# Kernel tuning notes

Hardware: AMD Instinct MI355X
Metric: run time of the kernel (lower is better)

The kernel has to match this reference:

```python
import jax, jax.numpy as jnp
import numpy as np
from jax import lax

B, H, W, C = 4, 96, 96, 256
F = 256
KH = KW = 3
K = KH * KW
DG = 1
CG = C // DG
SH = SW = 1
DH = DW = 1
PAD_T = (DH * (KH - 1)) // 2  # 'same' padding (top/left) for 3x3 dil 1
PAD_L = (DW * (KW - 1)) // 2


def setup_inputs() -> dict:
    key = jax.random.key(0)
    k1, k2, k3 = jax.random.split(key, 3)
    x = jax.random.normal(k1, (B, H, W, C), jnp.float32)
    # offset/mask conv weights (orig init zeros; small random to exercise sampling)
    om_kernel = jax.random.normal(k2, (KH, KW, C, DG * 3 * K), jnp.float32) * 0.01
    om_bias = jnp.zeros((DG * 3 * K,), jnp.float32)
    stdv = 1.0 / np.sqrt(C * KH * KW)
    kernel = jax.random.uniform(k3, (K * C, F), jnp.float32, -stdv, stdv)
    bias = jnp.zeros((F,), jnp.float32)
    return {"x": x, "om_kernel": om_kernel, "om_bias": om_bias, "kernel": kernel, "bias": bias}


def reference(x, om_kernel, om_bias, kernel, bias):
    Bx, Hx, Wx, Cx = x.shape
    # offset/mask prediction conv (NHWC, 'SAME', matches keras Conv2D)
    om = lax.conv_general_dilated(
        x, om_kernel, (SH, SW), "SAME", rhs_dilation=(DH, DW),
        dimension_numbers=("NHWC", "HWIO", "NHWC")) + om_bias
    Ho, Wo = om.shape[1], om.shape[2]
    off = om[..., : 2 * DG * K].reshape(Bx, Ho, Wo, DG, K, 2)  # (dy, dx) per group/kpoint
    mask = jax.nn.sigmoid(om[..., 2 * DG * K :]).reshape(Bx, Ho, Wo, DG, K) * 2.0

    # base sampling grid: y = ho*SH - PAD_T + ki*DH (+ dy), similarly x
    base_y = (jnp.arange(Ho) * SH - PAD_T)[:, None] + (jnp.arange(KH) * DH)[None, :]  # [Ho,KH]
    base_x = (jnp.arange(Wo) * SW - PAD_L)[:, None] + (jnp.arange(KW) * DW)[None, :]  # [Wo,KW]
    gy = jnp.broadcast_to(base_y[:, None, :, None], (Ho, Wo, KH, KW)).reshape(Ho, Wo, K)
    gx = jnp.broadcast_to(base_x[None, :, None, :], (Ho, Wo, KH, KW)).reshape(Ho, Wo, K)

    py = gy[None, :, :, None, :].astype(x.dtype) + off[..., 0]  # [B,Ho,Wo,DG,K]
    px = gx[None, :, :, None, :].astype(x.dtype) + off[..., 1]

    # reorder to [B, N, DG] with N = Ho*Wo*K (K varies fastest after spatial)
    N = Ho * Wo * K
    py = py.transpose(0, 1, 2, 4, 3).reshape(Bx, N, DG)
    px = px.transpose(0, 1, 2, 4, 3).reshape(Bx, N, DG)
    mask_t = mask.transpose(0, 1, 2, 4, 3).reshape(Bx, N, DG)

    y0 = jnp.floor(py)
    x0 = jnp.floor(px)
    fy = py - y0
    fx = px - x0

    xf = x.reshape(Bx, Hx * Wx, DG, CG)
    val = jnp.zeros((Bx, N, DG, CG), x.dtype)
    for yi, wy in ((y0, 1.0 - fy), (y0 + 1.0, fy)):
        for xi, wx in ((x0, 1.0 - fx), (x0 + 1.0, fx)):
            valid = (yi >= 0) & (yi < Hx) & (xi >= 0) & (xi < Wx)
            yc = jnp.clip(yi, 0, Hx - 1).astype(jnp.int32)
            xc = jnp.clip(xi, 0, Wx - 1).astype(jnp.int32)
            lin = yc * Wx + xc  # [B,N,DG]
            g = jnp.take_along_axis(xf, lin[..., None], axis=1)  # [B,N,DG,CG]
            val = val + g * (wy * wx * valid.astype(x.dtype))[..., None]

    # modulate and im2col -> GEMM
    cols = (val * mask_t[..., None]).reshape(Bx, Ho * Wo, K * Cx)
    out = jnp.matmul(cols, kernel).reshape(Bx, Ho, Wo, -1) + bias
    return out
```

## Files before the change

kernel.cpp:

```cpp
#include <hip/hip_runtime.h>
#include <hip/hip_bf16.h>
#include <stdint.h>
#include <stddef.h>


namespace {
constexpr int H  = 96, W = 96, C = 256, F = 256;
constexpr int HP = 98;
constexpr int NP = 4 * 96 * 96;
constexpr int KC = 9 * 256;

constexpr int NB_PAD  = 4 * HP * HP / 8;
constexpr int NB_OMW  = 9 * 32;
constexpr int NB_WT   = (KC / 64) * (F / 64);
}

typedef __attribute__((ext_vector_type(8))) short bf16x8;
typedef __attribute__((ext_vector_type(4))) float floatx4;

__device__ __forceinline__ void load_lds16(const void* g, void* l) {
  __builtin_amdgcn_global_load_lds((const __attribute__((address_space(1))) void*)g,
                                   (__attribute__((address_space(3))) void*)l,
                                   16, 0, 0);
}

__device__ __forceinline__ uint32_t pk2(float lo, float hi) {
  __hip_bfloat162 t = __float22bfloat162_rn(float2{lo, hi});
  return *reinterpret_cast<uint32_t*>(&t);
}

__device__ __forceinline__ void acc8(uint4 v, float w, float* a) {
  a[0] += w * __uint_as_float(v.x << 16); a[1] += w * __uint_as_float(v.x & 0xffff0000u);
  a[2] += w * __uint_as_float(v.y << 16); a[3] += w * __uint_as_float(v.y & 0xffff0000u);
  a[4] += w * __uint_as_float(v.z << 16); a[5] += w * __uint_as_float(v.z & 0xffff0000u);
  a[6] += w * __uint_as_float(v.w << 16); a[7] += w * __uint_as_float(v.w & 0xffff0000u);
}

__global__ __launch_bounds__(256) void k_pad(const float* __restrict__ x,
                                             uint4* __restrict__ xp4) {
  const int tid = threadIdx.x;
  const int sub = tid >> 5, cid = tid & 31;
  const int pp  = blockIdx.x * 8 + sub;
  const int b   = pp / (HP * HP);
  const int r   = pp % (HP * HP);
  const int y   = r / HP, xq = r % HP;
  uint4 o = {0u, 0u, 0u, 0u};
  if (y >= 1 && y <= H && xq >= 1 && xq <= W) {
    const float* src = x + ((size_t)((b * H + (y - 1)) * W + (xq - 1))) * C + cid * 8;
    const float4 v0 = *(const float4*)src;
    const float4 v1 = *(const float4*)(src + 4);
    o.x = pk2(v0.x, v0.y); o.y = pk2(v0.z, v0.w);
    o.z = pk2(v1.x, v1.y); o.w = pk2(v1.z, v1.w);
  }
  xp4[(size_t)pp * 32 + cid] = o;
}

__global__ __launch_bounds__(256) void k_wprep(const float* __restrict__ omk,
                                               const float* __restrict__ kern,
                                               __hip_bfloat16* __restrict__ wom,
                                               __hip_bfloat16* __restrict__ wt) {
  __shared__ float t[64][65];
  const int bi = blockIdx.x, tid = threadIdx.x;

  if (bi < NB_OMW) {
    const int kk = bi / 32, oc = bi % 32;
    float v = (oc < 27) ? omk[(size_t)(kk * 256 + tid) * 27 + oc] : 0.f;
    wom[(size_t)oc * KC + kk * 256 + tid] = __float2bfloat16(v);
  } else {
    const int j   = bi - NB_OMW;
    const int kc0 = (j % (KC / 64)) * 64, f0 = (j / (KC / 64)) * 64;
    const int rr = tid >> 6, cc = tid & 63;
#pragma unroll
    for (int i = 0; i < 16; ++i)
      t[rr * 16 + i][cc] = kern[(size_t)(kc0 + rr * 16 + i) * F + f0 + cc];
    __syncthreads();
#pragma unroll
    for (int i = 0; i < 16; ++i) {
      const int frow = rr * 16 + i;
      wt[(size_t)(f0 + frow) * KC + kc0 + cc] = __float2bfloat16(t[cc][frow]);
    }
  }
}

__global__ __launch_bounds__(256) void k_omgemm(const __hip_bfloat16* __restrict__ xp,
                                                const __hip_bfloat16* __restrict__ wom,
                                                float* __restrict__ pOm) {
  __shared__ __align__(16) char lds[12288];
  const int tid  = threadIdx.x;
  const int xr   = blockIdx.x;
  const int xs   = (xr & 7) * 72 + (xr >> 3);
  const int m0   = xs * 64;
  const int lane = tid & 63, wave = tid >> 6;
  const int quad = lane >> 4, l16 = lane & 15;

  const int kp  = (tid & 3) ^ ((tid >> 3) & 3);
  const int row = tid >> 2;
  {
  }
  const int p  = m0 + row;
  const int b  = p / (H * W);
  const int hw = p % (H * W);
  const int h  = hw / W, w = hw % W;
  const __hip_bfloat16* abase = xp + ((size_t)(b * HP + h) * HP + w) * C + kp * 8;
  const __hip_bfloat16* bbase = wom + (size_t)row * KC + kp * 8;

  auto stage = [&](int buf, int k0) {
    const int kk = k0 >> 8, c0 = k0 & 255;
    const int aoff = ((kk / 3) * HP + (kk % 3)) * C + c0;
    char* base = &lds[buf * 6144];
    load_lds16(abase + aoff, base + tid * 16);
    if (tid < 128) load_lds16(bbase + k0, base + 4096 + tid * 16);
  };

  floatx4 acc[2];
  acc[0] = (floatx4){0.f, 0.f, 0.f, 0.f};
  acc[1] = (floatx4){0.f, 0.f, 0.f, 0.f};

  const int swq = (quad ^ ((l16 >> 1) & 3)) * 16;

  stage(0, 0);
  int cur = 0;
#pragma unroll 1
  for (int k0 = 0; k0 < KC; k0 += 32) {
    __syncthreads();
    if (k0 + 32 < KC) stage(cur ^ 1, k0 + 32);
    const char* base = &lds[cur * 6144];

    bf16x8 af = *(const bf16x8*)&base[(wave * 16 + l16) * 64 + swq];
    bf16x8 b0 = *(const bf16x8*)&base[4096 + (l16) * 64 + swq];
    bf16x8 b1 = *(const bf16x8*)&base[4096 + (16 + l16) * 64 + swq];
    acc[0] = __builtin_amdgcn_mfma_f32_16x16x32_bf16(af, b0, acc[0], 0, 0, 0);
    acc[1] = __builtin_amdgcn_mfma_f32_16x16x32_bf16(af, b1, acc[1], 0, 0, 0);
    cur ^= 1;
  }

#pragma unroll
  for (int nt = 0; nt < 2; ++nt) {
    const int gm = m0 + wave * 16 + quad * 4;
    const int gn = nt * 16 + l16;
#pragma unroll
    for (int r = 0; r < 4; ++r)
      pOm[(size_t)(gm + r) * 32 + gn] = acc[nt][r];
  }
}

__global__ __launch_bounds__(256) void k_sample(const uint4* __restrict__ xp4,
                                                const float* __restrict__ pOm,
                                                const float* __restrict__ om_bias,
                                                uint4* __restrict__ cols4) {
  __shared__ float2 s_ow[8][9][4];

  const int tid = threadIdx.x;
  const int sub = tid >> 5, cid = tid & 31;
  const int bs  = (blockIdx.x & 7) * 576 + (blockIdx.x >> 3);

  if (tid < 72) {
    const int ps = tid / 9, k = tid % 9;
    const int p  = bs * 8 + ps;
    const int b  = p / (H * W);
    const int hw = p % (H * W);
    const int h = hw / W, w = hw % W;
    const float dy = om_bias[2 * k]     + pOm[(size_t)p * 32 + 2 * k];
    const float dx = om_bias[2 * k + 1] + pOm[(size_t)p * 32 + 2 * k + 1];
    const float mv = om_bias[18 + k]    + pOm[(size_t)p * 32 + 18 + k];
    const float m  = 2.f / (1.f + __expf(-mv));
    const float sy = (float)(h - 1 + k / 3) + dy;
    const float sx = (float)(w - 1 + k % 3) + dx;
    const float y0f = floorf(sy), x0f = floorf(sx);
    const float fy = sy - y0f, fx = sx - x0f;
    const int y0 = (int)y0f, x0 = (int)x0f;
#pragma unroll
    for (int c2 = 0; c2 < 4; ++c2) {
      const int dy2 = c2 >> 1, dx2 = c2 & 1;
      const int yi = y0 + dy2, xi = x0 + dx2;
      const bool valid = (yi >= 0) & (yi < H) & (xi >= 0) & (xi < W);
      const float wgt = valid ? (dy2 ? fy : 1.f - fy) * (dx2 ? fx : 1.f - fx) * m : 0.f;
      const int yc = min(max(yi + 1, 0), HP - 1);
      const int xc = min(max(xi + 1, 0), HP - 1);
      const int off = ((b * HP + yc) * HP + xc) * 32;
      s_ow[ps][k][c2] = float2{__int_as_float(off), wgt};
    }
  }
  __syncthreads();

  const int p = bs * 8 + sub;
  uint4* __restrict__ ob = cols4 + (size_t)p * 288 + cid;

#pragma unroll 1
  for (int k = 0; k < 9; ++k) {
    const float2 ow0 = s_ow[sub][k][0], ow1 = s_ow[sub][k][1];
    const float2 ow2 = s_ow[sub][k][2], ow3 = s_ow[sub][k][3];
    float a[8] = {0.f, 0.f, 0.f, 0.f, 0.f, 0.f, 0.f, 0.f};
    acc8(xp4[(size_t)__float_as_int(ow0.x) + cid], ow0.y, a);
    acc8(xp4[(size_t)__float_as_int(ow1.x) + cid], ow1.y, a);
    acc8(xp4[(size_t)__float_as_int(ow2.x) + cid], ow2.y, a);
    acc8(xp4[(size_t)__float_as_int(ow3.x) + cid], ow3.y, a);
    uint4 o;
    o.x = pk2(a[0], a[1]); o.y = pk2(a[2], a[3]);
    o.z = pk2(a[4], a[5]); o.w = pk2(a[6], a[7]);
    ob[k * 32] = o;
  }
}

__global__ __launch_bounds__(256) void k_gemm(const __hip_bfloat16* __restrict__ A,
                                              const __hip_bfloat16* __restrict__ Bt,
                                              const float* __restrict__ bias,
                                              float* __restrict__ out) {
  __shared__ __align__(16) char lds[28672];

  const int tid  = threadIdx.x;
  const int m0   = blockIdx.x * 96;
  const int n0   = blockIdx.y * 128;
  const int lane = tid & 63, wave = tid >> 6;
  const int wm = wave & 1, wn = wave >> 1;
  const int quad = lane >> 4, l16 = lane & 15;

  const int row = tid >> 2, kp = (tid & 3) ^ ((tid >> 3) & 3);
  const __hip_bfloat16* a0 = A  + (size_t)(m0 + row) * KC + kp * 8;
  const __hip_bfloat16* a1 = A  + (size_t)(m0 + 64 + row) * KC + kp * 8;
  const __hip_bfloat16* b0 = Bt + (size_t)(n0 + row) * KC + kp * 8;
  const __hip_bfloat16* b1 = Bt + (size_t)(n0 + 64 + row) * KC + kp * 8;

  auto stage = [&](int buf, int k0) {
    char* base = &lds[buf * 14336];
    load_lds16(a0 + k0, base + tid * 16);
    if (tid < 128) load_lds16(a1 + k0, base + 4096 + tid * 16);
    load_lds16(b0 + k0, base + 6144 + tid * 16);
    load_lds16(b1 + k0, base + 10240 + tid * 16);
  };

  floatx4 acc[3][4];
#pragma unroll
  for (int i = 0; i < 3; ++i)
#pragma unroll
    for (int j = 0; j < 4; ++j) acc[i][j] = (floatx4){0.f, 0.f, 0.f, 0.f};

  const int swq = (quad ^ ((l16 >> 1) & 3)) * 16;

  stage(0, 0);
  int cur = 0;
#pragma unroll 1
  for (int k0 = 0; k0 < KC; k0 += 32) {
    __syncthreads();
    if (k0 + 32 < KC) stage(cur ^ 1, k0 + 32);
    const char* base = &lds[cur * 14336];

    bf16x8 af[3], bfr[4];
#pragma unroll
    for (int mt = 0; mt < 3; ++mt)
      af[mt] = *(const bf16x8*)&base[(wm * 48 + mt * 16 + l16) * 64 + swq];
#pragma unroll
    for (int nt = 0; nt < 4; ++nt)
      bfr[nt] = *(const bf16x8*)&base[6144 + (wn * 64 + nt * 16 + l16) * 64 + swq];
#pragma unroll
    for (int mt = 0; mt < 3; ++mt)
#pragma unroll
      for (int nt = 0; nt < 4; ++nt)
        acc[mt][nt] = __builtin_amdgcn_mfma_f32_16x16x32_bf16(af[mt], bfr[nt], acc[mt][nt], 0, 0, 0);
    cur ^= 1;
  }

#pragma unroll
  for (int mt = 0; mt < 3; ++mt) {
#pragma unroll
    for (int nt = 0; nt < 4; ++nt) {
      const int gm = m0 + wm * 48 + mt * 16 + quad * 4;
      const int gn = n0 + wn * 64 + nt * 16 + l16;
      const float bs = bias[gn];
#pragma unroll
      for (int r = 0; r < 4; ++r)
        out[(size_t)(gm + r) * F + gn] = acc[mt][nt][r] + bs;
    }
  }
}

extern "C" void kernel_launch(void* const* d_in, const int* in_sizes, int n_in,
                              void* d_out, int out_size, void* d_ws, size_t ws_size,
                              hipStream_t stream) {
  const float* x    = (const float*)d_in[0];
  const float* omk  = (const float*)d_in[1];
  const float* omb  = (const float*)d_in[2];
  const float* kern = (const float*)d_in[3];
  const float* bias = (const float*)d_in[4];
  float* out = (float*)d_out;

  char* ws = (char*)d_ws;
  size_t off = 0;
  __hip_bfloat16* wt   = (__hip_bfloat16*)(ws + off); off += (size_t)F * KC * 2;
  __hip_bfloat16* xp   = (__hip_bfloat16*)(ws + off); off += (size_t)4 * HP * HP * C * 2;
  __hip_bfloat16* wom  = (__hip_bfloat16*)(ws + off); off += (size_t)32 * KC * 2;
  float*          pOm  = (float*)(ws + off);          off += (size_t)NP * 32 * 4;
  __hip_bfloat16* cols = (__hip_bfloat16*)(ws + off);

  k_pad   <<<dim3(NB_PAD),           256, 0, stream>>>(x, (uint4*)xp);
  k_wprep <<<dim3(NB_OMW + NB_WT),   256, 0, stream>>>(omk, kern, wom, wt);
  k_omgemm<<<dim3(576),              256, 0, stream>>>(xp, wom, pOm);
  k_sample<<<dim3(NP / 8),           256, 0, stream>>>((const uint4*)xp, pOm, omb, (uint4*)cols);
  k_gemm  <<<dim3(NP / 96, F / 128), 256, 0, stream>>>(cols, wt, bias, out);
}
```

Measured before the change: 213.0 us.

## Deepen omgemm K-step to 128 and swizzle gemm block order for L2 locality

The offset/mask conv GEMM now stages 128-wide K slices, four MFMA pairs per barrier instead of one, in a larger double-buffered LDS area with an XOR-swizzled 16-chunk row layout. This cuts the number of __syncthreads and stage issues per output tile. The main GEMM moves from a 2D grid to a 1D grid of 768 blocks, remapped so that neighbouring blocks share A rows and both N halves. That mapping is meant to improve L2/MALL reuse. The larger LDS footprint (48KB) may lower occupancy for the omgemm kernel.

```diff
diff --git a/kernel.cpp b/kernel.cpp
--- a/kernel.cpp
+++ b/kernel.cpp
@@ -85,7 +85,7 @@
 __global__ __launch_bounds__(256) void k_omgemm(const __hip_bfloat16* __restrict__ xp,
                                                 const __hip_bfloat16* __restrict__ wom,
                                                 float* __restrict__ pOm) {
-  __shared__ __align__(16) char lds[12288];
+  __shared__ __align__(16) char lds[49152];
   const int tid  = threadIdx.x;
   const int xr   = blockIdx.x;
   const int xs   = (xr & 7) * 72 + (xr >> 3);
@@ -93,44 +93,56 @@
   const int lane = tid & 63, wave = tid >> 6;
   const int quad = lane >> 4, l16 = lane & 15;
 
-  const int kp  = (tid & 3) ^ ((tid >> 3) & 3);
-  const int row = tid >> 2;
-  {
-  }
-  const int p  = m0 + row;
-  const int b  = p / (H * W);
-  const int hw = p % (H * W);
-  const int h  = hw / W, w = hw % W;
-  const __hip_bfloat16* abase = xp + ((size_t)(b * HP + h) * HP + w) * C + kp * 8;
-  const __hip_bfloat16* bbase = wom + (size_t)row * KC + kp * 8;
+  const int srow = tid >> 4;
+  const int gchk = (tid & 15) ^ srow;
+
+  const __hip_bfloat16* abase[4];
+#pragma unroll
+  for (int j = 0; j < 4; ++j) {
+    const int p  = m0 + srow + j * 16;
+    const int b  = p / (H * W);
+    const int hw = p % (H * W);
+    const int h  = hw / W, w = hw % W;
+    abase[j] = xp + ((size_t)(b * HP + h) * HP + w) * C + gchk * 8;
+  }
+  const __hip_bfloat16* bbase[2];
+#pragma unroll
+  for (int j = 0; j < 2; ++j)
+    bbase[j] = wom + (size_t)(srow + j * 16) * KC + gchk * 8;
 
   auto stage = [&](int buf, int k0) {
     const int kk = k0 >> 8, c0 = k0 & 255;
     const int aoff = ((kk / 3) * HP + (kk % 3)) * C + c0;
-    char* base = &lds[buf * 6144];
-    load_lds16(abase + aoff, base + tid * 16);
-    if (tid < 128) load_lds16(bbase + k0, base + 4096 + tid * 16);
+    char* base = &lds[buf * 24576];
+#pragma unroll
+    for (int j = 0; j < 4; ++j)
+      load_lds16(abase[j] + aoff, base + j * 4096 + tid * 16);
+#pragma unroll
+    for (int j = 0; j < 2; ++j)
+      load_lds16(bbase[j] + k0, base + 16384 + j * 4096 + tid * 16);
   };
 
   floatx4 acc[2];
   acc[0] = (floatx4){0.f, 0.f, 0.f, 0.f};
   acc[1] = (floatx4){0.f, 0.f, 0.f, 0.f};
 
-  const int swq = (quad ^ ((l16 >> 1) & 3)) * 16;
-
   stage(0, 0);
   int cur = 0;
 #pragma unroll 1
-  for (int k0 = 0; k0 < KC; k0 += 32) {
+  for (int k0 = 0; k0 < KC; k0 += 128) {
     __syncthreads();
-    if (k0 + 32 < KC) stage(cur ^ 1, k0 + 32);
-    const char* base = &lds[cur * 6144];
-
-    bf16x8 af = *(const bf16x8*)&base[(wave * 16 + l16) * 64 + swq];
-    bf16x8 b0 = *(const bf16x8*)&base[4096 + (l16) * 64 + swq];
-    bf16x8 b1 = *(const bf16x8*)&base[4096 + (16 + l16) * 64 + swq];
-    acc[0] = __builtin_amdgcn_mfma_f32_16x16x32_bf16(af, b0, acc[0], 0, 0, 0);
-    acc[1] = __builtin_amdgcn_mfma_f32_16x16x32_bf16(af, b1, acc[1], 0, 0, 0);
+    if (k0 + 128 < KC) stage(cur ^ 1, k0 + 128);
+    const char* base = &lds[cur * 24576];
+
+#pragma unroll
+    for (int ks = 0; ks < 4; ++ks) {
+      const int slot = (((ks * 4 + quad) ^ l16) & 15) * 16;
+      bf16x8 af = *(const bf16x8*)&base[(wave * 16 + l16) * 256 + slot];
+      bf16x8 b0 = *(const bf16x8*)&base[16384 + l16 * 256 + slot];
+      bf16x8 b1 = *(const bf16x8*)&base[16384 + (16 + l16) * 256 + slot];
+      acc[0] = __builtin_amdgcn_mfma_f32_16x16x32_bf16(af, b0, acc[0], 0, 0, 0);
+      acc[1] = __builtin_amdgcn_mfma_f32_16x16x32_bf16(af, b1, acc[1], 0, 0, 0);
+    }
     cur ^= 1;
   }
 
@@ -209,8 +221,9 @@
   __shared__ __align__(16) char lds[28672];
 
   const int tid  = threadIdx.x;
-  const int m0   = blockIdx.x * 96;
-  const int n0   = blockIdx.y * 128;
+  const int u    = (blockIdx.x & 7) * 96 + (blockIdx.x >> 3);
+  const int m0   = (u >> 1) * 96;
+  const int n0   = (u & 1) * 128;
   const int lane = tid & 63, wave = tid >> 6;
   const int wm = wave & 1, wn = wave >> 1;
   const int quad = lane >> 4, l16 = lane & 15;
@@ -292,9 +305,9 @@
   float*          pOm  = (float*)(ws + off);          off += (size_t)NP * 32 * 4;
   __hip_bfloat16* cols = (__hip_bfloat16*)(ws + off);
 
-  k_pad   <<<dim3(NB_PAD),           256, 0, stream>>>(x, (uint4*)xp);
-  k_wprep <<<dim3(NB_OMW + NB_WT),   256, 0, stream>>>(omk, kern, wom, wt);
-  k_omgemm<<<dim3(576),              256, 0, stream>>>(xp, wom, pOm);
-  k_sample<<<dim3(NP / 8),           256, 0, stream>>>((const uint4*)xp, pOm, omb, (uint4*)cols);
-  k_gemm  <<<dim3(NP / 96, F / 128), 256, 0, stream>>>(cols, wt, bias, out);
-}
+  k_pad   <<<dim3(NB_PAD),         256, 0, stream>>>(x, (uint4*)xp);
+  k_wprep <<<dim3(NB_OMW + NB_WT), 256, 0, stream>>>(omk, kern, wom, wt);
+  k_omgemm<<<dim3(576),            256, 0, stream>>>(xp, wom, pOm);
+  k_sample<<<dim3(NP / 8),         256, 0, stream>>>((const uint4*)xp, pOm, omb, (uint4*)cols);
+  k_gemm  <<<dim3(768),            256, 0, stream>>>(cols, wt, bias, out);
+}
```

Result: faster. 201.4 us (-5.4%).
